# Performance work log

Measured on AMD Instinct MI355X. Metric: run time of the kernel, lower is better.

The kernel has to match this reference:

```python
import jax, jax.numpy as jnp
import numpy as np

B, L, D = 2, 4096, 1024
H, HD = 16, D // 16
W = 256          # window_size
C = 256          # chunk/block size (== W, so each block sees prev + current block)
NC = L // C
SCALE = HD ** -0.5


def complex_linear(z, Wr, Wi):
    # z: [..., D, 2]; W*: [out, in] (torch Linear convention y = x @ W^T)
    xr, xi = z[..., 0], z[..., 1]
    yr = jnp.einsum('...i,oi->...o', xr, Wr) - jnp.einsum('...i,oi->...o', xi, Wi)
    yi = jnp.einsum('...i,oi->...o', xr, Wi) + jnp.einsum('...i,oi->...o', xi, Wr)
    return jnp.stack([yr, yi], axis=-1)


def _heads(x):
    # [B, L, D, 2] -> [B, H, NC, C, HD, 2]
    return x.reshape(B, L, H, HD, 2).transpose(0, 2, 1, 3, 4).reshape(B, H, NC, C, HD, 2)


def _band_mask():
    # block c, query local qi (global i = c*C + qi), key local kj over [prev block | cur block]
    # global j = (c-1)*C + kj ; valid iff 0 <= j <= i and i - j < W
    c = jnp.arange(NC)[:, None, None]
    qi = jnp.arange(C)[None, :, None]
    kj = jnp.arange(2 * C)[None, None, :]
    i = c * C + qi
    j = (c - 1) * C + kj
    return (j >= 0) & (j <= i) & (i - j < W)  # [NC, C, 2C]


def setup_inputs() -> dict:
    key = jax.random.key(0)
    ks = jax.random.split(key, 9)
    s = D ** -0.5
    inp = {'z': jax.random.normal(ks[0], (B, L, D, 2), jnp.float32)}
    names = ['Wq_r', 'Wq_i', 'Wk_r', 'Wk_i', 'Wv_r', 'Wv_i', 'Wo_r', 'Wo_i']
    for n, k in zip(names, ks[1:]):
        inp[n] = jax.random.normal(k, (D, D), jnp.float32) * s
    return inp


def reference(z, Wq_r, Wq_i, Wk_r, Wk_i, Wv_r, Wv_i, Wo_r, Wo_i):
    q = _heads(complex_linear(z, Wq_r, Wq_i))  # [B,H,NC,C,HD,2]
    k = _heads(complex_linear(z, Wk_r, Wk_i))
    v = _heads(complex_linear(z, Wv_r, Wv_i))

    def with_prev(x):  # [B,H,NC,C,HD,2] -> [B,H,NC,2C,HD,2] (prev block | cur block)
        prev = jnp.concatenate([jnp.zeros_like(x[:, :, :1]), x[:, :, :-1]], axis=2)
        return jnp.concatenate([prev, x], axis=3)

    kc = with_prev(k)
    vc = with_prev(v)

    # Re(q * conj(k)) = qr*kr + qi*ki
    scores = (jnp.einsum('bhncd,bhnkd->bhnck', q[..., 0], kc[..., 0])
              + jnp.einsum('bhncd,bhnkd->bhnck', q[..., 1], kc[..., 1])) * SCALE
    scores = jnp.where(_band_mask()[None, None], scores, -jnp.inf)
    w = jax.nn.softmax(scores, axis=-1)  # [B,H,NC,C,2C]

    out_r = jnp.einsum('bhnck,bhnkd->bhncd', w, vc[..., 0])
    out_i = jnp.einsum('bhnck,bhnkd->bhncd', w, vc[..., 1])
    out = jnp.stack([out_r, out_i], axis=-1)           # [B,H,NC,C,HD,2]
    out = out.reshape(B, H, L, HD, 2).transpose(0, 2, 1, 3, 4).reshape(B, L, D, 2)
    return complex_linear(out, Wo_r, Wo_i)
```

## Files before the change

kernel.cpp:

```cpp
#include <hip/hip_runtime.h>
#include <hip/hip_bf16.h>
#include <stdint.h>


typedef __attribute__((ext_vector_type(8))) short bf16x8;
typedef __attribute__((ext_vector_type(8))) unsigned short u16x8;
typedef __attribute__((ext_vector_type(4))) float f32x4;

#define PA_SCALE 0.125f
#define UNR _Pragma("unroll")

__device__ __forceinline__ unsigned short f2bf(float f) {
  unsigned int u = __builtin_bit_cast(unsigned int, f);
  u += 0x7fffu + ((u >> 16) & 1u);
  return (unsigned short)(u >> 16);
}

#define GLD16(gp, lp)                                          \
  __builtin_amdgcn_global_load_lds(                            \
      (const __attribute__((address_space(1))) void*)(gp),     \
      (__attribute__((address_space(3))) void*)(lp), 16, 0, 0)

__global__ __launch_bounds__(256) void pa_pack_A(const float* __restrict__ z,
                                                 unsigned short* __restrict__ A1) {
  int idx = (blockIdx.x * 256 + threadIdx.x) * 8;
  int m = idx >> 10, d = idx & 1023;
  const float2* zp = (const float2*)z + idx;
  u16x8 re, im;
  UNR for (int j = 0; j < 8; ++j) {
    float2 f = zp[j];
    re[j] = f2bf(f.x);
    im[j] = f2bf(f.y);
  }
  *(u16x8*)(A1 + (size_t)m * 2048 + d)        = re;
  *(u16x8*)(A1 + (size_t)m * 2048 + 1024 + d) = im;
}

__global__ __launch_bounds__(256) void pa_pack_B(
    const float* __restrict__ Wq_r, const float* __restrict__ Wq_i,
    const float* __restrict__ Wk_r, const float* __restrict__ Wk_i,
    const float* __restrict__ Wv_r, const float* __restrict__ Wv_i,
    const float* __restrict__ Wo_r, const float* __restrict__ Wo_i,
    unsigned short* __restrict__ Bp) {
  int idx = (blockIdx.x * 256 + threadIdx.x) * 8;
  int n = idx >> 10, d = idx & 1023;
  int proj = n >> 11, part = (n >> 10) & 1, o = n & 1023;
  const float* Wr; const float* Wi;
  if (proj == 0)      { Wr = Wq_r; Wi = Wq_i; }
  else if (proj == 1) { Wr = Wk_r; Wi = Wk_i; }
  else if (proj == 2) { Wr = Wv_r; Wi = Wv_i; }
  else                { Wr = Wo_r; Wi = Wo_i; }
  const float* pr = Wr + (size_t)o * 1024 + d;
  const float* pi = Wi + (size_t)o * 1024 + d;
  u16x8 lo, hi;
  UNR for (int j = 0; j < 8; ++j) {
    float r = pr[j], im = pi[j];
    if (part == 0) { lo[j] = f2bf(r);  hi[j] = f2bf(-im); }
    else           { lo[j] = f2bf(im); hi[j] = f2bf(r);  }
  }
  *(u16x8*)(Bp + (size_t)n * 2048 + d)        = lo;
  *(u16x8*)(Bp + (size_t)n * 2048 + 1024 + d) = hi;
}

#define BARR()                              \
  do {                                      \
    __builtin_amdgcn_s_barrier();           \
    __builtin_amdgcn_sched_barrier(0);      \
  } while (0)

#define READ_A(P, MH)                                                         \
  UNR for (int i = 0; i < 4; ++i)                                             \
    UNR for (int ks = 0; ks < 2; ++ks)                                        \
      af[i][ks] = *(const bf16x8*)&lds[P][MH][aoff + i * 1024 +               \
                                              ((ks * 32 + koff) ^ cxor)];

#define READ_B(P, NH, DST)                                                    \
  UNR for (int j = 0; j < 2; ++j)                                             \
    UNR for (int ks = 0; ks < 2; ++ks)                                        \
      DST[j][ks] = *(const bf16x8*)&lds[P][2 + (NH)][boff + j * 1024 +        \
                                                     ((ks * 32 + koff) ^ cxor)];

#define MFMA_Q(MB, NB, BF)                                                    \
  UNR for (int ks = 0; ks < 2; ++ks)                                          \
    UNR for (int i = 0; i < 4; ++i)                                           \
      UNR for (int j = 0; j < 2; ++j)                                         \
        acc[(MB) + i][(NB) + j] = __builtin_amdgcn_mfma_f32_16x16x32_bf16(    \
            af[i][ks], BF[j][ks], acc[(MB) + i][(NB) + j], 0, 0, 0);

#define TILE(P, T)                                                            \
  {                                                                           \
    READ_A(P, 0);                                                             \
    READ_B(P, 0, b0);                                                         \
    stageB(0, (T) + 1);                                                       \
    BARR();                                                                   \
    __builtin_amdgcn_s_setprio(1);                                            \
    MFMA_Q(0, 0, b0);                                                         \
    __builtin_amdgcn_s_setprio(0);                                            \
    BARR();                                                                   \
    READ_B(P, 1, b1);                                                         \
    stageA(0, (T) + 2);                                                       \
    BARR();                                                                   \
    __builtin_amdgcn_s_setprio(1);                                            \
    MFMA_Q(0, 2, b1);                                                         \
    __builtin_amdgcn_s_setprio(0);                                            \
    BARR();                                                                   \
    READ_A(P, 1);                                                             \
    stageB(1, (T) + 2);                                                       \
    BARR();                                                                   \
    __builtin_amdgcn_s_setprio(1);                                            \
    MFMA_Q(4, 2, b1);                                                         \
    __builtin_amdgcn_s_setprio(0);                                            \
    BARR();                                                                   \
    stageA(1, (T) + 2);                                                       \
    BARR();                                                                   \
    __builtin_amdgcn_s_setprio(1);                                            \
    MFMA_Q(4, 0, b0);                                                         \
    __builtin_amdgcn_s_setprio(0);                                            \
    asm volatile("s_waitcnt vmcnt(6)" ::: "memory");                          \
    __builtin_amdgcn_sched_barrier(0);                                        \
    BARR();                                                                   \
  }

template <int EPI>
__global__ __launch_bounds__(512, 2) void pa_gemm8(
    const unsigned short* __restrict__ A,
    const unsigned short* __restrict__ B,
    void* __restrict__ Cout, int K, int N) {
  __shared__ unsigned short lds[2][4][128 * 64];

  const int tid = threadIdx.x;
  const int lane = tid & 63, wid = tid >> 6;
  const int wm = wid >> 2, wn = wid & 3;
  const int lr = lane & 15, lh = lane >> 4;

  const int nwg = gridDim.x * gridDim.y;
  const int wg = blockIdx.y * gridDim.x + blockIdx.x;
  const int cpx = nwg >> 3;
  const int swz = (wg & 7) * cpx + (wg >> 3);
  const int bx = swz % gridDim.x, by = swz / gridDim.x;
  const int tm0 = by * 256, tn0 = bx * 256;

  const int NT = K >> 6;

  const int srow = lane >> 3;
  const int scolS = ((lane & 7) ^ srow) * 8;

  auto stageA = [&](int half, int ts) {
    int t = ts < NT ? ts : ts - NT;
    const unsigned short* g0 = A + (size_t)(tm0 + half * 128) * K + t * 64 + scolS;
    unsigned short* l0 = &lds[ts & 1][half][0];
    UNR for (int c = 0; c < 2; ++c) {
      int chunk = wid * 2 + c;
      GLD16(g0 + (size_t)(chunk * 8 + srow) * K, l0 + chunk * 512);
    }
  };
  auto stageB = [&](int half, int ts) {
    int t = ts < NT ? ts : ts - NT;
    const unsigned short* g0 = B + (size_t)(tn0 + half * 128) * K + t * 64 + scolS;
    unsigned short* l0 = &lds[ts & 1][2 + half][0];
    UNR for (int c = 0; c < 2; ++c) {
      int chunk = wid * 2 + c;
      GLD16(g0 + (size_t)(chunk * 8 + srow) * K, l0 + chunk * 512);
    }
  };

  const int aoff = (wm * 64 + lr) * 64;
  const int boff = (wn * 32 + lr) * 64;
  const int koff = lh * 8;
  const int cxor = (lr & 7) * 8;

  f32x4 acc[8][4];
  f32x4 zero4 = {0.f, 0.f, 0.f, 0.f};
  UNR for (int i = 0; i < 8; ++i)
    UNR for (int j = 0; j < 4; ++j) acc[i][j] = zero4;

  bf16x8 af[4][2], b0[2][2], b1[2][2];

  stageA(0, 0); stageB(0, 0); stageB(1, 0); stageA(1, 0);
  stageA(0, 1); stageB(1, 1); stageA(1, 1);
  asm volatile("s_waitcnt vmcnt(6)" ::: "memory");
  __builtin_amdgcn_sched_barrier(0);
  __builtin_amdgcn_s_barrier();
  __builtin_amdgcn_sched_barrier(0);

  for (int t = 0; t < NT; t += 2) {
    TILE(0, t);
    TILE(1, t + 1);
  }

  UNR for (int mh = 0; mh < 2; ++mh)
    UNR for (int i = 0; i < 4; ++i)
      UNR for (int nh = 0; nh < 2; ++nh)
        UNR for (int j = 0; j < 2; ++j)
          UNR for (int r = 0; r < 4; ++r) {
            int row = tm0 + mh * 128 + wm * 64 + i * 16 + lh * 4 + r;
            int col = tn0 + nh * 128 + wn * 32 + j * 16 + lr;
            float v = acc[mh * 4 + i][nh * 2 + j][r];
            if (EPI == 0) {
              ((unsigned short*)Cout)[(size_t)row * N + col] = f2bf(v);
            } else {
              int part = col >> 10, dd = col & 1023;
              ((float*)Cout)[((size_t)row * 1024 + dd) * 2 + part] = v;
            }
          }
}

#define QK1(SI)                                                               \
  UNR for (int kk = 0; kk < 2; ++kk)                                          \
    UNR for (int f = 0; f < 4; ++f) {                                         \
      bf16x8 br = *(const bf16x8*)&Ks[0][f * 16 + lr][kk * 32 + lh * 8];      \
      bf16x8 bi = *(const bf16x8*)&Ks[1][f * 16 + lr][kk * 32 + lh * 8];      \
      sac[SI][f] = __builtin_amdgcn_mfma_f32_16x16x32_bf16(qfr[kk], br,       \
                                                           sac[SI][f], 0, 0, 0); \
      sac[SI][f] = __builtin_amdgcn_mfma_f32_16x16x32_bf16(qfi[kk], bi,       \
                                                           sac[SI][f], 0, 0, 0); \
    }

__global__ __launch_bounds__(512) void pa_attn(const unsigned short* __restrict__ C1,
                                               unsigned short* __restrict__ A2) {
  __shared__ unsigned short Ks[2][64][72];
  __shared__ unsigned short Vts[6][2][64][72];
  __shared__ unsigned short Ps[8][16][72];

  int bid = blockIdx.x;
  int half = bid & 1, nc = (bid >> 1) & 15, h = (bid >> 5) & 15, b = bid >> 9;
  int tid = threadIdx.x;
  int l = tid & 63, wv = tid >> 6;
  int lr = l & 15, lh = l >> 4;
  int base = wv >> 2;

  const int C1LD = 6144;
  const int rowB = b * 4096;
  const int colQr = h * 64,        colQi = 1024 + h * 64;
  const int colKr = 2048 + h * 64, colKi = 3072 + h * 64;
  const int colVr = 4096 + h * 64, colVi = 5120 + h * 64;
  const int q0 = half * 128;
  const int qw = q0 + wv * 16;

  bf16x8 qfr[2], qfi[2];
  {
    const unsigned short* pr = C1 + (size_t)(rowB + nc * 256 + qw + lr) * C1LD + colQr;
    const unsigned short* pi = C1 + (size_t)(rowB + nc * 256 + qw + lr) * C1LD + colQi;
    qfr[0] = *(const bf16x8*)(pr + lh * 8);
    qfr[1] = *(const bf16x8*)(pr + 32 + lh * 8);
    qfi[0] = *(const bf16x8*)(pi + lh * 8);
    qfi[1] = *(const bf16x8*)(pi + 32 + lh * 8);
  }

  f32x4 zero4 = {0.f, 0.f, 0.f, 0.f};
  f32x4 sac[5][4];
#pragma unroll
  for (int c = 0; c < 5; ++c)
#pragma unroll
    for (int f = 0; f < 4; ++f) sac[c][f] = zero4;

#pragma unroll
  for (int c = 0; c < 6; ++c) {
    __syncthreads();
#pragma unroll
    for (int s = 0; s < 2; ++s) {
      int seg = s * 512 + tid;
      int arr = seg >> 9, row = (seg >> 3) & 63, sg = seg & 7;
      int kj = q0 + c * 64 + row;
      int tok = (nc - 1) * 256 + kj; if (tok < 0) tok = 0;
      const unsigned short* rp = C1 + (size_t)(rowB + tok) * C1LD;
      *(bf16x8*)&Ks[arr][row][sg * 8] =
          *(const bf16x8*)(rp + (arr ? colKi : colKr) + sg * 8);
      bf16x8 v = *(const bf16x8*)(rp + (arr ? colVi : colVr) + sg * 8);
#pragma unroll
      for (int j = 0; j < 8; ++j) Vts[c][arr][sg * 8 + j][row] = (unsigned short)v[j];
    }
    __syncthreads();
    if (wv < 4) { if (c < 5) { QK1(c); } }
    else        { if (c >= 1) { QK1(c - 1); } }
  }

  float mx[4] = {-1e30f, -1e30f, -1e30f, -1e30f};
#pragma unroll
  for (int si = 0; si < 5; ++si)
#pragma unroll
    for (int f = 0; f < 4; ++f)
#pragma unroll
      for (int r = 0; r < 4; ++r) {
        int qi_ = qw + lh * 4 + r;
        int kj  = q0 + (si + base) * 64 + f * 16 + lr;
        bool valid = (kj > qi_) && (kj <= qi_ + 256) && (nc > 0 || kj >= 256);
        float s = valid ? sac[si][f][r] * PA_SCALE : -1e30f;
        sac[si][f][r] = s;
        mx[r] = fmaxf(mx[r], s);
      }
#pragma unroll
  for (int r = 0; r < 4; ++r)
#pragma unroll
    for (int d = 1; d < 16; d <<= 1) mx[r] = fmaxf(mx[r], __shfl_xor(mx[r], d));

  float sm[4] = {0.f, 0.f, 0.f, 0.f};
#pragma unroll
  for (int si = 0; si < 5; ++si)
#pragma unroll
    for (int f = 0; f < 4; ++f)
#pragma unroll
      for (int r = 0; r < 4; ++r) {
        float p = __expf(sac[si][f][r] - mx[r]);
        sac[si][f][r] = p;
        sm[r] += p;
      }
#pragma unroll
  for (int r = 0; r < 4; ++r)
#pragma unroll
    for (int d = 1; d < 16; d <<= 1) sm[r] += __shfl_xor(sm[r], d);
  float inv[4];
#pragma unroll
  for (int r = 0; r < 4; ++r) inv[r] = 1.0f / sm[r];

  f32x4 oac[2][4];
#pragma unroll
  for (int p = 0; p < 2; ++p)
#pragma unroll
    for (int f = 0; f < 4; ++f) oac[p][f] = zero4;

  const unsigned short* vb = &Vts[0][0][0][0] + base * 9216;

#pragma unroll
  for (int si = 0; si < 5; ++si) {
#pragma unroll
    for (int f = 0; f < 4; ++f)
#pragma unroll
      for (int r = 0; r < 4; ++r)
        Ps[wv][lh * 4 + r][f * 16 + lr] = f2bf(sac[si][f][r]);

    bf16x8 pa0 = *(const bf16x8*)&Ps[wv][lr][lh * 8];
    bf16x8 pa1 = *(const bf16x8*)&Ps[wv][lr][32 + lh * 8];
#pragma unroll
    for (int kk = 0; kk < 2; ++kk) {
      bf16x8 pak = kk ? pa1 : pa0;
#pragma unroll
      for (int fc = 0; fc < 4; ++fc) {
        const unsigned short* pvr =
            vb + si * 9216 + (fc * 16 + lr) * 72 + kk * 32 + lh * 8;
        bf16x8 vr = *(const bf16x8*)pvr;
        bf16x8 vi = *(const bf16x8*)(pvr + 4608);
        oac[0][fc] = __builtin_amdgcn_mfma_f32_16x16x32_bf16(pak, vr, oac[0][fc], 0, 0, 0);
        oac[1][fc] = __builtin_amdgcn_mfma_f32_16x16x32_bf16(pak, vi, oac[1][fc], 0, 0, 0);
      }
    }
  }

#pragma unroll
  for (int fc = 0; fc < 4; ++fc)
#pragma unroll
    for (int r = 0; r < 4; ++r) {
      int m  = rowB + nc * 256 + qw + lh * 4 + r;
      int hd = fc * 16 + lr;
      A2[(size_t)m * 2048 + h * 64 + hd]        = f2bf(oac[0][fc][r] * inv[r]);
      A2[(size_t)m * 2048 + 1024 + h * 64 + hd] = f2bf(oac[1][fc][r] * inv[r]);
    }
}

extern "C" void kernel_launch(void* const* d_in, const int* in_sizes, int n_in,
                              void* d_out, int out_size, void* d_ws, size_t ws_size,
                              hipStream_t stream) {
  const float* z = (const float*)d_in[0];
  unsigned short* A1 = (unsigned short*)d_ws;
  unsigned short* Bp = (unsigned short*)((char*)d_ws + 33554432ull);
  unsigned short* C1 = (unsigned short*)((char*)d_ws + 67108864ull);
  float* out = (float*)d_out;

  pa_pack_A<<<4096, 256, 0, stream>>>(z, A1);
  pa_pack_B<<<4096, 256, 0, stream>>>(
      (const float*)d_in[1], (const float*)d_in[2],
      (const float*)d_in[3], (const float*)d_in[4],
      (const float*)d_in[5], (const float*)d_in[6],
      (const float*)d_in[7], (const float*)d_in[8], Bp);
  pa_gemm8<0><<<dim3(24, 32), 512, 0, stream>>>(A1, Bp, C1, 2048, 6144);
  pa_attn<<<1024, 512, 0, stream>>>(C1, A1);
  pa_gemm8<1><<<dim3(8, 32), 512, 0, stream>>>(A1, Bp + (size_t)6144 * 2048, out,
                                               2048, 2048);
}
```

Measured before the change: 389.0 us.

## Fuse pack kernels, stream attention per chunk without max, interleave output weights

```diff
diff --git a/kernel.cpp b/kernel.cpp
--- a/kernel.cpp
+++ b/kernel.cpp
@@ -21,45 +21,47 @@
       (const __attribute__((address_space(1))) void*)(gp),     \
       (__attribute__((address_space(3))) void*)(lp), 16, 0, 0)
 
-__global__ __launch_bounds__(256) void pa_pack_A(const float* __restrict__ z,
-                                                 unsigned short* __restrict__ A1) {
-  int idx = (blockIdx.x * 256 + threadIdx.x) * 8;
-  int m = idx >> 10, d = idx & 1023;
-  const float2* zp = (const float2*)z + idx;
-  u16x8 re, im;
-  UNR for (int j = 0; j < 8; ++j) {
-    float2 f = zp[j];
-    re[j] = f2bf(f.x);
-    im[j] = f2bf(f.y);
-  }
-  *(u16x8*)(A1 + (size_t)m * 2048 + d)        = re;
-  *(u16x8*)(A1 + (size_t)m * 2048 + 1024 + d) = im;
-}
-
-__global__ __launch_bounds__(256) void pa_pack_B(
+__global__ __launch_bounds__(256) void pa_pack(
+    const float* __restrict__ z,
     const float* __restrict__ Wq_r, const float* __restrict__ Wq_i,
     const float* __restrict__ Wk_r, const float* __restrict__ Wk_i,
     const float* __restrict__ Wv_r, const float* __restrict__ Wv_i,
     const float* __restrict__ Wo_r, const float* __restrict__ Wo_i,
-    unsigned short* __restrict__ Bp) {
-  int idx = (blockIdx.x * 256 + threadIdx.x) * 8;
-  int n = idx >> 10, d = idx & 1023;
-  int proj = n >> 11, part = (n >> 10) & 1, o = n & 1023;
-  const float* Wr; const float* Wi;
-  if (proj == 0)      { Wr = Wq_r; Wi = Wq_i; }
-  else if (proj == 1) { Wr = Wk_r; Wi = Wk_i; }
-  else if (proj == 2) { Wr = Wv_r; Wi = Wv_i; }
-  else                { Wr = Wo_r; Wi = Wo_i; }
-  const float* pr = Wr + (size_t)o * 1024 + d;
-  const float* pi = Wi + (size_t)o * 1024 + d;
-  u16x8 lo, hi;
-  UNR for (int j = 0; j < 8; ++j) {
-    float r = pr[j], im = pi[j];
-    if (part == 0) { lo[j] = f2bf(r);  hi[j] = f2bf(-im); }
-    else           { lo[j] = f2bf(im); hi[j] = f2bf(r);  }
-  }
-  *(u16x8*)(Bp + (size_t)n * 2048 + d)        = lo;
-  *(u16x8*)(Bp + (size_t)n * 2048 + 1024 + d) = hi;
+    unsigned short* __restrict__ A1, unsigned short* __restrict__ Bp) {
+  int bid = blockIdx.x, tid = threadIdx.x;
+  if (bid < 4096) {
+    int idx = (bid * 256 + tid) * 8;
+    int m = idx >> 10, d = idx & 1023;
+    const float2* zp = (const float2*)z + idx;
+    u16x8 re, im;
+    UNR for (int j = 0; j < 8; ++j) {
+      float2 f = zp[j];
+      re[j] = f2bf(f.x);
+      im[j] = f2bf(f.y);
+    }
+    *(u16x8*)(A1 + (size_t)m * 2048 + d)        = re;
+    *(u16x8*)(A1 + (size_t)m * 2048 + 1024 + d) = im;
+  } else {
+    int idx = ((bid - 4096) * 256 + tid) * 8;
+    int n = idx >> 10, d = idx & 1023;
+    int proj = n >> 11, part = (n >> 10) & 1, o = n & 1023;
+    const float* Wr; const float* Wi;
+    if (proj == 0)      { Wr = Wq_r; Wi = Wq_i; }
+    else if (proj == 1) { Wr = Wk_r; Wi = Wk_i; }
+    else if (proj == 2) { Wr = Wv_r; Wi = Wv_i; }
+    else                { Wr = Wo_r; Wi = Wo_i; }
+    const float* pr = Wr + (size_t)o * 1024 + d;
+    const float* pi = Wi + (size_t)o * 1024 + d;
+    u16x8 lo, hi;
+    UNR for (int j = 0; j < 8; ++j) {
+      float r = pr[j], im = pi[j];
+      if (part == 0) { lo[j] = f2bf(r);  hi[j] = f2bf(-im); }
+      else           { lo[j] = f2bf(im); hi[j] = f2bf(r);  }
+    }
+    size_t nn = (proj < 3) ? (size_t)n : (size_t)(6144 + o * 2 + part);
+    *(u16x8*)(Bp + nn * 2048 + d)        = lo;
+    *(u16x8*)(Bp + nn * 2048 + 1024 + d) = hi;
+  }
 }
 
 #define BARR()                              \
@@ -199,27 +201,15 @@
             if (EPI == 0) {
               ((unsigned short*)Cout)[(size_t)row * N + col] = f2bf(v);
             } else {
-              int part = col >> 10, dd = col & 1023;
-              ((float*)Cout)[((size_t)row * 1024 + dd) * 2 + part] = v;
+              ((float*)Cout)[(size_t)row * N + col] = v;
             }
           }
 }
 
-#define QK1(SI)                                                               \
-  UNR for (int kk = 0; kk < 2; ++kk)                                          \
-    UNR for (int f = 0; f < 4; ++f) {                                         \
-      bf16x8 br = *(const bf16x8*)&Ks[0][f * 16 + lr][kk * 32 + lh * 8];      \
-      bf16x8 bi = *(const bf16x8*)&Ks[1][f * 16 + lr][kk * 32 + lh * 8];      \
-      sac[SI][f] = __builtin_amdgcn_mfma_f32_16x16x32_bf16(qfr[kk], br,       \
-                                                           sac[SI][f], 0, 0, 0); \
-      sac[SI][f] = __builtin_amdgcn_mfma_f32_16x16x32_bf16(qfi[kk], bi,       \
-                                                           sac[SI][f], 0, 0, 0); \
-    }
-
-__global__ __launch_bounds__(512) void pa_attn(const unsigned short* __restrict__ C1,
-                                               unsigned short* __restrict__ A2) {
+__global__ __launch_bounds__(512, 4) void pa_attn(const unsigned short* __restrict__ C1,
+                                                  unsigned short* __restrict__ A2) {
   __shared__ unsigned short Ks[2][64][72];
-  __shared__ unsigned short Vts[6][2][64][72];
+  __shared__ unsigned short Vts[2][64][72];
   __shared__ unsigned short Ps[8][16][72];
 
   int bid = blockIdx.x;
@@ -227,7 +217,6 @@
   int tid = threadIdx.x;
   int l = tid & 63, wv = tid >> 6;
   int lr = l & 15, lh = l >> 4;
-  int base = wv >> 2;
 
   const int C1LD = 6144;
   const int rowB = b * 4096;
@@ -248,11 +237,12 @@
   }
 
   f32x4 zero4 = {0.f, 0.f, 0.f, 0.f};
-  f32x4 sac[5][4];
-#pragma unroll
-  for (int c = 0; c < 5; ++c)
-#pragma unroll
-    for (int f = 0; f < 4; ++f) sac[c][f] = zero4;
+  float sm[4] = {0.f, 0.f, 0.f, 0.f};
+  f32x4 oac[2][4];
+#pragma unroll
+  for (int p = 0; p < 2; ++p)
+#pragma unroll
+    for (int f = 0; f < 4; ++f) oac[p][f] = zero4;
 
 #pragma unroll
   for (int c = 0; c < 6; ++c) {
@@ -268,43 +258,57 @@
           *(const bf16x8*)(rp + (arr ? colKi : colKr) + sg * 8);
       bf16x8 v = *(const bf16x8*)(rp + (arr ? colVi : colVr) + sg * 8);
 #pragma unroll
-      for (int j = 0; j < 8; ++j) Vts[c][arr][sg * 8 + j][row] = (unsigned short)v[j];
+      for (int j = 0; j < 8; ++j) Vts[arr][sg * 8 + j][row] = (unsigned short)v[j];
     }
     __syncthreads();
-    if (wv < 4) { if (c < 5) { QK1(c); } }
-    else        { if (c >= 1) { QK1(c - 1); } }
-  }
-
-  float mx[4] = {-1e30f, -1e30f, -1e30f, -1e30f};
-#pragma unroll
-  for (int si = 0; si < 5; ++si)
-#pragma unroll
-    for (int f = 0; f < 4; ++f)
-#pragma unroll
-      for (int r = 0; r < 4; ++r) {
-        int qi_ = qw + lh * 4 + r;
-        int kj  = q0 + (si + base) * 64 + f * 16 + lr;
-        bool valid = (kj > qi_) && (kj <= qi_ + 256) && (nc > 0 || kj >= 256);
-        float s = valid ? sac[si][f][r] * PA_SCALE : -1e30f;
-        sac[si][f][r] = s;
-        mx[r] = fmaxf(mx[r], s);
+
+    bool active = (wv < 4) ? (c < 5) : (c >= 1);
+    if (active) {
+      f32x4 sl[4];
+#pragma unroll
+      for (int f = 0; f < 4; ++f) sl[f] = zero4;
+      __builtin_amdgcn_s_setprio(1);
+#pragma unroll
+      for (int kk = 0; kk < 2; ++kk)
+#pragma unroll
+        for (int f = 0; f < 4; ++f) {
+          bf16x8 br = *(const bf16x8*)&Ks[0][f * 16 + lr][kk * 32 + lh * 8];
+          bf16x8 bi = *(const bf16x8*)&Ks[1][f * 16 + lr][kk * 32 + lh * 8];
+          sl[f] = __builtin_amdgcn_mfma_f32_16x16x32_bf16(qfr[kk], br, sl[f], 0, 0, 0);
+          sl[f] = __builtin_amdgcn_mfma_f32_16x16x32_bf16(qfi[kk], bi, sl[f], 0, 0, 0);
+        }
+      __builtin_amdgcn_s_setprio(0);
+
+#pragma unroll
+      for (int f = 0; f < 4; ++f)
+#pragma unroll
+        for (int r = 0; r < 4; ++r) {
+          int qi_ = qw + lh * 4 + r;
+          int kj  = q0 + c * 64 + f * 16 + lr;
+          bool valid = (kj > qi_) && (kj <= qi_ + 256) && (nc > 0 || kj >= 256);
+          float p = valid ? __expf(sl[f][r] * PA_SCALE) : 0.f;
+          sm[r] += p;
+          Ps[wv][lh * 4 + r][f * 16 + lr] = f2bf(p);
+        }
+
+      bf16x8 pa0 = *(const bf16x8*)&Ps[wv][lr][lh * 8];
+      bf16x8 pa1 = *(const bf16x8*)&Ps[wv][lr][32 + lh * 8];
+      __builtin_amdgcn_s_setprio(1);
+#pragma unroll
+      for (int kk = 0; kk < 2; ++kk) {
+        bf16x8 pak = kk ? pa1 : pa0;
+#pragma unroll
+        for (int fc = 0; fc < 4; ++fc) {
+          bf16x8 vr = *(const bf16x8*)&Vts[0][fc * 16 + lr][kk * 32 + lh * 8];
+          bf16x8 vi = *(const bf16x8*)&Vts[1][fc * 16 + lr][kk * 32 + lh * 8];
+          oac[0][fc] = __builtin_amdgcn_mfma_f32_16x16x32_bf16(pak, vr, oac[0][fc], 0, 0, 0);
+          oac[1][fc] = __builtin_amdgcn_mfma_f32_16x16x32_bf16(pak, vi, oac[1][fc], 0, 0, 0);
+        }
       }
-#pragma unroll
-  for (int r = 0; r < 4; ++r)
-#pragma unroll
-    for (int d = 1; d < 16; d <<= 1) mx[r] = fmaxf(mx[r], __shfl_xor(mx[r], d));
-
-  float sm[4] = {0.f, 0.f, 0.f, 0.f};
-#pragma unroll
-  for (int si = 0; si < 5; ++si)
-#pragma unroll
-    for (int f = 0; f < 4; ++f)
-#pragma unroll
-      for (int r = 0; r < 4; ++r) {
-        float p = __expf(sac[si][f][r] - mx[r]);
-        sac[si][f][r] = p;
-        sm[r] += p;
-      }
+      __builtin_amdgcn_s_setprio(0);
+    }
+  }
+
 #pragma unroll
   for (int r = 0; r < 4; ++r)
 #pragma unroll
@@ -312,39 +316,6 @@
   float inv[4];
 #pragma unroll
   for (int r = 0; r < 4; ++r) inv[r] = 1.0f / sm[r];
-
-  f32x4 oac[2][4];
-#pragma unroll
-  for (int p = 0; p < 2; ++p)
-#pragma unroll
-    for (int f = 0; f < 4; ++f) oac[p][f] = zero4;
-
-  const unsigned short* vb = &Vts[0][0][0][0] + base * 9216;
-
-#pragma unroll
-  for (int si = 0; si < 5; ++si) {
-#pragma unroll
-    for (int f = 0; f < 4; ++f)
-#pragma unroll
-      for (int r = 0; r < 4; ++r)
-        Ps[wv][lh * 4 + r][f * 16 + lr] = f2bf(sac[si][f][r]);
-
-    bf16x8 pa0 = *(const bf16x8*)&Ps[wv][lr][lh * 8];
-    bf16x8 pa1 = *(const bf16x8*)&Ps[wv][lr][32 + lh * 8];
-#pragma unroll
-    for (int kk = 0; kk < 2; ++kk) {
-      bf16x8 pak = kk ? pa1 : pa0;
-#pragma unroll
-      for (int fc = 0; fc < 4; ++fc) {
-        const unsigned short* pvr =
-            vb + si * 9216 + (fc * 16 + lr) * 72 + kk * 32 + lh * 8;
-        bf16x8 vr = *(const bf16x8*)pvr;
-        bf16x8 vi = *(const bf16x8*)(pvr + 4608);
-        oac[0][fc] = __builtin_amdgcn_mfma_f32_16x16x32_bf16(pak, vr, oac[0][fc], 0, 0, 0);
-        oac[1][fc] = __builtin_amdgcn_mfma_f32_16x16x32_bf16(pak, vi, oac[1][fc], 0, 0, 0);
-      }
-    }
-  }
 
 #pragma unroll
   for (int fc = 0; fc < 4; ++fc)
@@ -366,12 +337,12 @@
   unsigned short* C1 = (unsigned short*)((char*)d_ws + 67108864ull);
   float* out = (float*)d_out;
 
-  pa_pack_A<<<4096, 256, 0, stream>>>(z, A1);
-  pa_pack_B<<<4096, 256, 0, stream>>>(
+  pa_pack<<<8192, 256, 0, stream>>>(
+      z,
       (const float*)d_in[1], (const float*)d_in[2],
       (const float*)d_in[3], (const float*)d_in[4],
       (const float*)d_in[5], (const float*)d_in[6],
-      (const float*)d_in[7], (const float*)d_in[8], Bp);
+      (const float*)d_in[7], (const float*)d_in[8], A1, Bp);
   pa_gemm8<0><<<dim3(24, 32), 512, 0, stream>>>(A1, Bp, C1, 2048, 6144);
   pa_attn<<<1024, 512, 0, stream>>>(C1, A1);
   pa_gemm8<1><<<dim3(8, 32), 512, 0, stream>>>(A1, Bp + (size_t)6144 * 2048, out,
```

After: 368.2 us. 1.06x faster.
